# Performance work log

Hardware: AMD Instinct MI355X
Metric: run time of the kernel (lower is better)

Reference implementation:

```python
import jax, jax.numpy as jnp
import numpy as np
from math import sqrt

N_HEADS = 8

def setup_inputs() -> dict:
    key = jax.random.key(0)
    k1, k2, k3 = jax.random.split(key, 3)
    B, S, D = 2, 2048, 512
    X = jax.random.normal(k1, (B, S, D), dtype=jnp.float32)
    # kaiming_normal for (fan_in = D) -> std = sqrt(2/D)
    Wq = jax.random.normal(k2, (D, D), dtype=jnp.float32) * jnp.float32(sqrt(2.0 / D))
    Wv = jax.random.normal(k3, (D, 1), dtype=jnp.float32) * jnp.float32(sqrt(2.0 / D))
    return {"X": X, "Wq": Wq, "Wv": Wv}

def reference(X, Wq, Wv):
    B, S, D = X.shape
    H = N_HEADS
    dh = D // H
    # Q: (B, H, S, dh)
    Q = (X @ Wq).reshape(B, S, H, dh).transpose(0, 2, 1, 3)
    # NOTE: original uses L2 norm (NOT squared) in the 'distance' expression; be faithful.
    n = jnp.linalg.norm(Q, axis=-1, keepdims=True)          # (B,H,S,1)
    dots = jnp.einsum('bhsd,bhtd->bhst', Q, Q)              # (B,H,S,S)
    scores = -(n - 2.0 * dots + jnp.swapaxes(n, -2, -1)) / jnp.float32(sqrt(dh))
    P = jax.nn.softmax(scores, axis=-1)                     # (B,H,S,S)
    # Wh: (H, D, dh); Ah = Wh @ Wh^T : (H, D, D)
    Wh = Wq.reshape(D, H, dh).transpose(1, 0, 2)
    Ah = jnp.einsum('hij,hkj->hik', Wh, Wh)
    PX = jnp.einsum('bhst,btd->bhsd', P, X)                 # (B,H,S,D)
    attn_scores = jnp.einsum('bhsd,hde->bhse', PX, Ah)      # (B,H,S,D)
    applied = attn_scores @ Wv                              # (B,H,S,1)
    # GumbelSigmoid in eval mode (deterministic): plain sigmoid of logits.
    selection = jax.nn.sigmoid(applied)
    return selection
```

## Files before the change

kernel.cpp:

```cpp
#include <hip/hip_runtime.h>


typedef __attribute__((ext_vector_type(8))) short bf16x8;
typedef __attribute__((ext_vector_type(4))) float f32x4;

#if __has_builtin(__builtin_amdgcn_exp2f)
#define EXP2F(x) __builtin_amdgcn_exp2f(x)
#else
#define EXP2F(x) exp2f(x)
#endif

#define LOG2E 1.44269504088896341f
#define C025  (0.25f * LOG2E)
#define C0125 (0.125f * LOG2E)

__device__ inline unsigned int f2b(float f) {
    unsigned int u = __float_as_uint(f);
    return (u + 0x7fffu + ((u >> 16) & 1u)) >> 16;
}

#define SWZ(row, c) ((row) * 64 + (((c) ^ ((row) & 7)) * 8))

__global__ __launch_bounds__(256) void qgemm_k(const float* __restrict__ X,
                                               const float* __restrict__ Wq,
                                               const float* __restrict__ Wv,
                                               unsigned short* __restrict__ Qh,
                                               float* __restrict__ nl_out,
                                               float* __restrict__ y_out) {
    __shared__ __align__(16) unsigned short As[64 * 64];
    __shared__ __align__(16) unsigned short Bs[64 * 64];
    __shared__ float tsh[256];
    int tid = threadIdx.x;
    int bid = blockIdx.x;
    int h = bid >> 6;
    int m0 = (bid & 63) * 64;
    int n0 = h * 64;
    int w = tid >> 6, lane = tid & 63;
    int tt = lane & 15, quad = lane >> 4;

    int arow = tid >> 3, achk = tid & 7;
    int bc = tid & 63, bjg = tid >> 6;

    const float* Xa0 = &X[(m0 + arow) * 512 + achk * 8];
    const float* Xa1 = Xa0 + 32 * 512;
    const float* Wb  = &Wq[n0 + bc];

    float4 a00, a01, a10, a11;
    float bv[16], wv[16];
    float tp = 0.f;
    f32x4 acc[4] = {{0.f,0.f,0.f,0.f},{0.f,0.f,0.f,0.f},
                    {0.f,0.f,0.f,0.f},{0.f,0.f,0.f,0.f}};

#define K1_LOADS(K0)                                                     \
    do {                                                                 \
        a00 = *(const float4*)&Xa0[(K0)];                                \
        a01 = *(const float4*)&Xa0[(K0) + 4];                            \
        a10 = *(const float4*)&Xa1[(K0)];                                \
        a11 = *(const float4*)&Xa1[(K0) + 4];                            \
        _Pragma("unroll")                                                \
        for (int i = 0; i < 8; ++i) {                                    \
            bv[i]     = Wb[((K0) + bjg * 8 + i) * 512];                  \
            bv[8 + i] = Wb[((K0) + (bjg + 4) * 8 + i) * 512];            \
            wv[i]     = Wv[(K0) + bjg * 8 + i];                          \
            wv[8 + i] = Wv[(K0) + (bjg + 4) * 8 + i];                    \
        }                                                                \
    } while (0)

    K1_LOADS(0);
    for (int k0 = 0; k0 < 512; k0 += 64) {
        __syncthreads();
        uint4 o;
        o.x = f2b(a00.x) | (f2b(a00.y) << 16);
        o.y = f2b(a00.z) | (f2b(a00.w) << 16);
        o.z = f2b(a01.x) | (f2b(a01.y) << 16);
        o.w = f2b(a01.z) | (f2b(a01.w) << 16);
        *(uint4*)&As[SWZ(arow, achk)] = o;
        o.x = f2b(a10.x) | (f2b(a10.y) << 16);
        o.y = f2b(a10.z) | (f2b(a10.w) << 16);
        o.z = f2b(a11.x) | (f2b(a11.y) << 16);
        o.w = f2b(a11.z) | (f2b(a11.w) << 16);
        *(uint4*)&As[SWZ(arow + 32, achk)] = o;
        o.x = f2b(bv[0]) | (f2b(bv[1]) << 16);
        o.y = f2b(bv[2]) | (f2b(bv[3]) << 16);
        o.z = f2b(bv[4]) | (f2b(bv[5]) << 16);
        o.w = f2b(bv[6]) | (f2b(bv[7]) << 16);
        *(uint4*)&Bs[SWZ(bc, bjg)] = o;
        o.x = f2b(bv[8])  | (f2b(bv[9])  << 16);
        o.y = f2b(bv[10]) | (f2b(bv[11]) << 16);
        o.z = f2b(bv[12]) | (f2b(bv[13]) << 16);
        o.w = f2b(bv[14]) | (f2b(bv[15]) << 16);
        *(uint4*)&Bs[SWZ(bc, bjg + 4)] = o;
        #pragma unroll
        for (int i = 0; i < 16; ++i) tp = fmaf(bv[i], wv[i], tp);
        __syncthreads();
        if (k0 < 448) K1_LOADS(k0 + 64);
        int ar = w * 16 + tt;
        bf16x8 fa0 = *(const bf16x8*)&As[SWZ(ar, quad)];
        bf16x8 fa1 = *(const bf16x8*)&As[SWZ(ar, quad + 4)];
        #pragma unroll
        for (int ct = 0; ct < 4; ++ct) {
            int br = ct * 16 + tt;
            bf16x8 fb0 = *(const bf16x8*)&Bs[SWZ(br, quad)];
            bf16x8 fb1 = *(const bf16x8*)&Bs[SWZ(br, quad + 4)];
            acc[ct] = __builtin_amdgcn_mfma_f32_16x16x32_bf16(fa0, fb0, acc[ct], 0, 0, 0);
            acc[ct] = __builtin_amdgcn_mfma_f32_16x16x32_bf16(fa1, fb1, acc[ct], 0, 0, 0);
        }
    }

    tsh[bjg * 64 + bc] = tp;
    __syncthreads();
    float tv[4];
    #pragma unroll
    for (int ct = 0; ct < 4; ++ct) {
        int c = ct * 16 + tt;
        tv[ct] = tsh[c] + tsh[64 + c] + tsh[128 + c] + tsh[192 + c];
    }

    float s2[4] = {0.f,0.f,0.f,0.f}, yp[4] = {0.f,0.f,0.f,0.f};
    #pragma unroll
    for (int ct = 0; ct < 4; ++ct)
        #pragma unroll
        for (int g = 0; g < 4; ++g) {
            float v = acc[ct][g];
            s2[g] = fmaf(v, v, s2[g]);
            yp[g] = fmaf(v, tv[ct], yp[g]);
            Qh[(m0 + w * 16 + quad * 4 + g) * 512 + n0 + ct * 16 + tt] =
                (unsigned short)f2b(v);
        }
    #pragma unroll
    for (int off = 1; off <= 8; off <<= 1)
        #pragma unroll
        for (int g = 0; g < 4; ++g) {
            s2[g] += __shfl_xor(s2[g], off);
            yp[g] += __shfl_xor(yp[g], off);
        }
    if (tt == 0) {
        int bb = m0 >> 11;
        #pragma unroll
        for (int g = 0; g < 4; ++g) {
            int row = m0 + w * 16 + quad * 4 + g;
            int idx = ((bb * 8 + h) << 11) + (row & 2047);
            nl_out[idx] = -C0125 * sqrtf(s2[g]);
            y_out[idx]  = yp[g];
        }
    }
}

__global__ __launch_bounds__(512, 4) void attn_k(const unsigned short* __restrict__ Qh,
                                                 const float* __restrict__ nl_in,
                                                 const float* __restrict__ y_in,
                                                 float* __restrict__ out) {
    __shared__ float redN[8][64];
    __shared__ float redD[8][64];
    int tid = threadIdx.x;
    int bid = blockIdx.x;
    int bh = bid & 15;
    int tile = bid >> 4;
    int s0 = tile * 64;
    int b = bh >> 3, h = bh & 7;
    const unsigned short* __restrict__ Qb = Qh + (size_t)(b * 2048) * 512 + h * 64;
    const float* __restrict__ nb = nl_in + bh * 2048;
    const float* __restrict__ yb = y_in + bh * 2048;
    int w = tid >> 6, lane = tid & 63;
    int tt = lane & 15, quad = lane >> 4;

    bf16x8 fa0[4], fa1[4];
    #pragma unroll
    for (int tl = 0; tl < 4; ++tl) {
        const unsigned short* r = &Qb[(size_t)(s0 + tl * 16 + tt) * 512];
        fa0[tl] = *(const bf16x8*)&r[quad * 8];
        fa1[tl] = *(const bf16x8*)&r[32 + quad * 8];
    }
    f32x4 num[4] = {{0.f,0.f,0.f,0.f},{0.f,0.f,0.f,0.f},
                    {0.f,0.f,0.f,0.f},{0.f,0.f,0.f,0.f}};
    f32x4 den[4] = {{0.f,0.f,0.f,0.f},{0.f,0.f,0.f,0.f},
                    {0.f,0.f,0.f,0.f},{0.f,0.f,0.f,0.f}};

    const unsigned short* rT = &Qb[(size_t)(w * 256 + tt) * 512];
    bf16x8 fb0c = *(const bf16x8*)&rT[quad * 8];
    bf16x8 fb1c = *(const bf16x8*)&rT[32 + quad * 8];
    float tqc = nb[w * 256 + tt];
    float yvc = yb[w * 256 + tt];
    for (int st = 0; st < 16; ++st) {
        bf16x8 fb0n, fb1n;
        float tqn = 0.f, yvn = 0.f;
        if (st < 15) {
            int tnext = w * 256 + (st + 1) * 16 + tt;
            const unsigned short* rN = &Qb[(size_t)tnext * 512];
            fb0n = *(const bf16x8*)&rN[quad * 8];
            fb1n = *(const bf16x8*)&rN[32 + quad * 8];
            tqn = nb[tnext];
            yvn = yb[tnext];
        }
        #pragma unroll
        for (int tl = 0; tl < 4; ++tl) {
            f32x4 dot = {0.f, 0.f, 0.f, 0.f};
            dot = __builtin_amdgcn_mfma_f32_16x16x32_bf16(fa0[tl], fb0c, dot, 0, 0, 0);
            dot = __builtin_amdgcn_mfma_f32_16x16x32_bf16(fa1[tl], fb1c, dot, 0, 0, 0);
            #pragma unroll
            for (int g = 0; g < 4; ++g) {
                float arg = fmaf(C025, dot[g], tqc);
                float e = EXP2F(arg);
                num[tl][g] = fmaf(e, yvc, num[tl][g]);
                den[tl][g] += e;
            }
        }
        if (st < 15) { fb0c = fb0n; fb1c = fb1n; tqc = tqn; yvc = yvn; }
    }

    #pragma unroll
    for (int off = 1; off <= 8; off <<= 1)
        #pragma unroll
        for (int tl = 0; tl < 4; ++tl)
            #pragma unroll
            for (int g = 0; g < 4; ++g) {
                num[tl][g] += __shfl_xor(num[tl][g], off);
                den[tl][g] += __shfl_xor(den[tl][g], off);
            }
    if (tt == 0) {
        #pragma unroll
        for (int tl = 0; tl < 4; ++tl)
            #pragma unroll
            for (int g = 0; g < 4; ++g) {
                redN[w][tl * 16 + quad * 4 + g] = num[tl][g];
                redD[w][tl * 16 + quad * 4 + g] = den[tl][g];
            }
    }
    __syncthreads();
    if (tid < 64) {
        float xn = 0.f, xd = 0.f;
        #pragma unroll
        for (int ww = 0; ww < 8; ++ww) {
            xn += redN[ww][tid];
            xd += redD[ww][tid];
        }
        float x = xn / xd;
        out[bh * 2048 + s0 + tid] = 1.0f / (1.0f + EXP2F(-x * LOG2E));
    }
}

extern "C" void kernel_launch(void* const* d_in, const int* in_sizes, int n_in,
                              void* d_out, int out_size, void* d_ws, size_t ws_size,
                              hipStream_t stream) {
    const float* X  = (const float*)d_in[0];
    const float* Wq = (const float*)d_in[1];
    const float* Wv = (const float*)d_in[2];
    float* ws = (float*)d_ws;

    float* nl_ws = ws;
    float* y_ws  = ws + 32768;
    unsigned short* Qh_ws = (unsigned short*)(ws + 65536);

    qgemm_k<<<512, 256, 0, stream>>>(X, Wq, Wv, Qh_ws, nl_ws, y_ws);
    attn_k<<<512, 512, 0, stream>>>(Qh_ws, nl_ws, y_ws, (float*)d_out);
}
```

Before: 96.97 us.

## Halve row tiles in GEMM and attention kernels to double grid parallelism

Both the Q projection kernel and the attention kernel switch from 64-row to 32-row tiles, doubling the number of blocks. In the GEMM the four waves now split the 32x64 output as 2x2 rather than one row strip each, which needs a new shared-memory reduction for the per-row norm and the Wv projection. The attention kernel's occupancy hint rises from 4 to 6. The aim is to fill more CUs and hide latency, at the cost of reloading the Wq tile and the key fragments twice as often.

```diff
diff --git a/kernel.cpp b/kernel.cpp
--- a/kernel.cpp
+++ b/kernel.cpp
@@ -21,42 +21,40 @@
 
 #define SWZ(row, c) ((row) * 64 + (((c) ^ ((row) & 7)) * 8))
 
-__global__ __launch_bounds__(256) void qgemm_k(const float* __restrict__ X,
-                                               const float* __restrict__ Wq,
-                                               const float* __restrict__ Wv,
-                                               unsigned short* __restrict__ Qh,
-                                               float* __restrict__ nl_out,
-                                               float* __restrict__ y_out) {
-    __shared__ __align__(16) unsigned short As[64 * 64];
+__global__ __launch_bounds__(256, 4) void qgemm_k(const float* __restrict__ X,
+                                                  const float* __restrict__ Wq,
+                                                  const float* __restrict__ Wv,
+                                                  unsigned short* __restrict__ Qh,
+                                                  float* __restrict__ nl_out,
+                                                  float* __restrict__ y_out) {
+    __shared__ __align__(16) unsigned short As[32 * 64];
     __shared__ __align__(16) unsigned short Bs[64 * 64];
     __shared__ float tsh[256];
+    __shared__ float redS[2][32], redY[2][32];
     int tid = threadIdx.x;
     int bid = blockIdx.x;
-    int h = bid >> 6;
-    int m0 = (bid & 63) * 64;
+    int h = bid >> 7;
+    int m0 = (bid & 127) * 32;
     int n0 = h * 64;
     int w = tid >> 6, lane = tid & 63;
     int tt = lane & 15, quad = lane >> 4;
+    int rh = w & 1, ch = w >> 1;
 
     int arow = tid >> 3, achk = tid & 7;
     int bc = tid & 63, bjg = tid >> 6;
 
-    const float* Xa0 = &X[(m0 + arow) * 512 + achk * 8];
-    const float* Xa1 = Xa0 + 32 * 512;
-    const float* Wb  = &Wq[n0 + bc];
-
-    float4 a00, a01, a10, a11;
+    const float* Xa = &X[(m0 + arow) * 512 + achk * 8];
+    const float* Wb = &Wq[n0 + bc];
+
+    float4 a0v, a1v;
     float bv[16], wv[16];
     float tp = 0.f;
-    f32x4 acc[4] = {{0.f,0.f,0.f,0.f},{0.f,0.f,0.f,0.f},
-                    {0.f,0.f,0.f,0.f},{0.f,0.f,0.f,0.f}};
+    f32x4 acc[2] = {{0.f,0.f,0.f,0.f},{0.f,0.f,0.f,0.f}};
 
 #define K1_LOADS(K0)                                                     \
     do {                                                                 \
-        a00 = *(const float4*)&Xa0[(K0)];                                \
-        a01 = *(const float4*)&Xa0[(K0) + 4];                            \
-        a10 = *(const float4*)&Xa1[(K0)];                                \
-        a11 = *(const float4*)&Xa1[(K0) + 4];                            \
+        a0v = *(const float4*)&Xa[(K0)];                                 \
+        a1v = *(const float4*)&Xa[(K0) + 4];                             \
         _Pragma("unroll")                                                \
         for (int i = 0; i < 8; ++i) {                                    \
             bv[i]     = Wb[((K0) + bjg * 8 + i) * 512];                  \
@@ -70,16 +68,11 @@
     for (int k0 = 0; k0 < 512; k0 += 64) {
         __syncthreads();
         uint4 o;
-        o.x = f2b(a00.x) | (f2b(a00.y) << 16);
-        o.y = f2b(a00.z) | (f2b(a00.w) << 16);
-        o.z = f2b(a01.x) | (f2b(a01.y) << 16);
-        o.w = f2b(a01.z) | (f2b(a01.w) << 16);
+        o.x = f2b(a0v.x) | (f2b(a0v.y) << 16);
+        o.y = f2b(a0v.z) | (f2b(a0v.w) << 16);
+        o.z = f2b(a1v.x) | (f2b(a1v.y) << 16);
+        o.w = f2b(a1v.z) | (f2b(a1v.w) << 16);
         *(uint4*)&As[SWZ(arow, achk)] = o;
-        o.x = f2b(a10.x) | (f2b(a10.y) << 16);
-        o.y = f2b(a10.z) | (f2b(a10.w) << 16);
-        o.z = f2b(a11.x) | (f2b(a11.y) << 16);
-        o.w = f2b(a11.z) | (f2b(a11.w) << 16);
-        *(uint4*)&As[SWZ(arow + 32, achk)] = o;
         o.x = f2b(bv[0]) | (f2b(bv[1]) << 16);
         o.y = f2b(bv[2]) | (f2b(bv[3]) << 16);
         o.z = f2b(bv[4]) | (f2b(bv[5]) << 16);
@@ -94,37 +87,37 @@
         for (int i = 0; i < 16; ++i) tp = fmaf(bv[i], wv[i], tp);
         __syncthreads();
         if (k0 < 448) K1_LOADS(k0 + 64);
-        int ar = w * 16 + tt;
+        int ar = rh * 16 + tt;
         bf16x8 fa0 = *(const bf16x8*)&As[SWZ(ar, quad)];
         bf16x8 fa1 = *(const bf16x8*)&As[SWZ(ar, quad + 4)];
         #pragma unroll
-        for (int ct = 0; ct < 4; ++ct) {
-            int br = ct * 16 + tt;
+        for (int c = 0; c < 2; ++c) {
+            int br = (ch * 2 + c) * 16 + tt;
             bf16x8 fb0 = *(const bf16x8*)&Bs[SWZ(br, quad)];
             bf16x8 fb1 = *(const bf16x8*)&Bs[SWZ(br, quad + 4)];
-            acc[ct] = __builtin_amdgcn_mfma_f32_16x16x32_bf16(fa0, fb0, acc[ct], 0, 0, 0);
-            acc[ct] = __builtin_amdgcn_mfma_f32_16x16x32_bf16(fa1, fb1, acc[ct], 0, 0, 0);
+            acc[c] = __builtin_amdgcn_mfma_f32_16x16x32_bf16(fa0, fb0, acc[c], 0, 0, 0);
+            acc[c] = __builtin_amdgcn_mfma_f32_16x16x32_bf16(fa1, fb1, acc[c], 0, 0, 0);
         }
     }
 
     tsh[bjg * 64 + bc] = tp;
     __syncthreads();
-    float tv[4];
-    #pragma unroll
-    for (int ct = 0; ct < 4; ++ct) {
-        int c = ct * 16 + tt;
-        tv[ct] = tsh[c] + tsh[64 + c] + tsh[128 + c] + tsh[192 + c];
+    float tv[2];
+    #pragma unroll
+    for (int c = 0; c < 2; ++c) {
+        int col = (ch * 2 + c) * 16 + tt;
+        tv[c] = tsh[col] + tsh[64 + col] + tsh[128 + col] + tsh[192 + col];
     }
 
     float s2[4] = {0.f,0.f,0.f,0.f}, yp[4] = {0.f,0.f,0.f,0.f};
     #pragma unroll
-    for (int ct = 0; ct < 4; ++ct)
+    for (int c = 0; c < 2; ++c)
         #pragma unroll
         for (int g = 0; g < 4; ++g) {
-            float v = acc[ct][g];
+            float v = acc[c][g];
             s2[g] = fmaf(v, v, s2[g]);
-            yp[g] = fmaf(v, tv[ct], yp[g]);
-            Qh[(m0 + w * 16 + quad * 4 + g) * 512 + n0 + ct * 16 + tt] =
+            yp[g] = fmaf(v, tv[c], yp[g]);
+            Qh[(m0 + rh * 16 + quad * 4 + g) * 512 + n0 + (ch * 2 + c) * 16 + tt] =
                 (unsigned short)f2b(v);
         }
     #pragma unroll
@@ -135,28 +128,35 @@
             yp[g] += __shfl_xor(yp[g], off);
         }
     if (tt == 0) {
-        int bb = m0 >> 11;
         #pragma unroll
         for (int g = 0; g < 4; ++g) {
-            int row = m0 + w * 16 + quad * 4 + g;
-            int idx = ((bb * 8 + h) << 11) + (row & 2047);
-            nl_out[idx] = -C0125 * sqrtf(s2[g]);
-            y_out[idx]  = yp[g];
-        }
-    }
-}
-
-__global__ __launch_bounds__(512, 4) void attn_k(const unsigned short* __restrict__ Qh,
+            redS[ch][rh * 16 + quad * 4 + g] = s2[g];
+            redY[ch][rh * 16 + quad * 4 + g] = yp[g];
+        }
+    }
+    __syncthreads();
+    if (tid < 32) {
+        float s = redS[0][tid] + redS[1][tid];
+        float y = redY[0][tid] + redY[1][tid];
+        int row = m0 + tid;
+        int bb = row >> 11;
+        int idx = ((bb * 8 + h) << 11) + (row & 2047);
+        nl_out[idx] = -C0125 * sqrtf(s);
+        y_out[idx]  = y;
+    }
+}
+
+__global__ __launch_bounds__(512, 6) void attn_k(const unsigned short* __restrict__ Qh,
                                                  const float* __restrict__ nl_in,
                                                  const float* __restrict__ y_in,
                                                  float* __restrict__ out) {
-    __shared__ float redN[8][64];
-    __shared__ float redD[8][64];
+    __shared__ float redN[8][32];
+    __shared__ float redD[8][32];
     int tid = threadIdx.x;
     int bid = blockIdx.x;
     int bh = bid & 15;
     int tile = bid >> 4;
-    int s0 = tile * 64;
+    int s0 = tile * 32;
     int b = bh >> 3, h = bh & 7;
     const unsigned short* __restrict__ Qb = Qh + (size_t)(b * 2048) * 512 + h * 64;
     const float* __restrict__ nb = nl_in + bh * 2048;
@@ -164,17 +164,15 @@
     int w = tid >> 6, lane = tid & 63;
     int tt = lane & 15, quad = lane >> 4;
 
-    bf16x8 fa0[4], fa1[4];
-    #pragma unroll
-    for (int tl = 0; tl < 4; ++tl) {
+    bf16x8 fa0[2], fa1[2];
+    #pragma unroll
+    for (int tl = 0; tl < 2; ++tl) {
         const unsigned short* r = &Qb[(size_t)(s0 + tl * 16 + tt) * 512];
         fa0[tl] = *(const bf16x8*)&r[quad * 8];
         fa1[tl] = *(const bf16x8*)&r[32 + quad * 8];
     }
-    f32x4 num[4] = {{0.f,0.f,0.f,0.f},{0.f,0.f,0.f,0.f},
-                    {0.f,0.f,0.f,0.f},{0.f,0.f,0.f,0.f}};
-    f32x4 den[4] = {{0.f,0.f,0.f,0.f},{0.f,0.f,0.f,0.f},
-                    {0.f,0.f,0.f,0.f},{0.f,0.f,0.f,0.f}};
+    f32x4 num[2] = {{0.f,0.f,0.f,0.f},{0.f,0.f,0.f,0.f}};
+    f32x4 den[2] = {{0.f,0.f,0.f,0.f},{0.f,0.f,0.f,0.f}};
 
     const unsigned short* rT = &Qb[(size_t)(w * 256 + tt) * 512];
     bf16x8 fb0c = *(const bf16x8*)&rT[quad * 8];
@@ -193,7 +191,7 @@
             yvn = yb[tnext];
         }
         #pragma unroll
-        for (int tl = 0; tl < 4; ++tl) {
+        for (int tl = 0; tl < 2; ++tl) {
             f32x4 dot = {0.f, 0.f, 0.f, 0.f};
             dot = __builtin_amdgcn_mfma_f32_16x16x32_bf16(fa0[tl], fb0c, dot, 0, 0, 0);
             dot = __builtin_amdgcn_mfma_f32_16x16x32_bf16(fa1[tl], fb1c, dot, 0, 0, 0);
@@ -211,7 +209,7 @@
     #pragma unroll
     for (int off = 1; off <= 8; off <<= 1)
         #pragma unroll
-        for (int tl = 0; tl < 4; ++tl)
+        for (int tl = 0; tl < 2; ++tl)
             #pragma unroll
             for (int g = 0; g < 4; ++g) {
                 num[tl][g] += __shfl_xor(num[tl][g], off);
@@ -219,7 +217,7 @@
             }
     if (tt == 0) {
         #pragma unroll
-        for (int tl = 0; tl < 4; ++tl)
+        for (int tl = 0; tl < 2; ++tl)
             #pragma unroll
             for (int g = 0; g < 4; ++g) {
                 redN[w][tl * 16 + quad * 4 + g] = num[tl][g];
@@ -227,7 +225,7 @@
             }
     }
     __syncthreads();
-    if (tid < 64) {
+    if (tid < 32) {
         float xn = 0.f, xd = 0.f;
         #pragma unroll
         for (int ww = 0; ww < 8; ++ww) {
@@ -251,6 +249,6 @@
     float* y_ws  = ws + 32768;
     unsigned short* Qh_ws = (unsigned short*)(ws + 65536);
 
-    qgemm_k<<<512, 256, 0, stream>>>(X, Wq, Wv, Qh_ws, nl_ws, y_ws);
-    attn_k<<<512, 512, 0, stream>>>(Qh_ws, nl_ws, y_ws, (float*)d_out);
-}
+    qgemm_k<<<1024, 256, 0, stream>>>(X, Wq, Wv, Qh_ws, nl_ws, y_ws);
+    attn_k<<<1024, 512, 0, stream>>>(Qh_ws, nl_ws, y_ws, (float*)d_out);
+}
```

New measurement: 151.0 us. +55.7%, slower.
